# Performance work log

Measured on AMD Instinct MI355X. Metric: run time of the kernel, lower is better.

## Reference

```python
import jax, jax.numpy as jnp
import numpy as np

H = 16        # num query heads
HKV = 4       # num kv heads
D = 128       # head_dim
HID = 2048    # hidden_size
G = H // HKV  # heads per kv group


def setup_inputs() -> dict:
    key = jax.random.key(0)
    ks = jax.random.split(key, 9)
    s = 0.02
    x = jax.random.normal(ks[0], (2, 2048, HID), dtype=jnp.float32)
    wq = jax.random.normal(ks[1], (HID, H * D), dtype=jnp.float32) * s
    bq = jnp.zeros((H * D,), jnp.float32)
    wk = jax.random.normal(ks[2], (HID, HKV * D), dtype=jnp.float32) * s
    bk = jnp.zeros((HKV * D,), jnp.float32)
    wv = jax.random.normal(ks[3], (HID, HKV * D), dtype=jnp.float32) * s
    bv = jnp.zeros((HKV * D,), jnp.float32)
    wo = jax.random.normal(ks[4], (HID, HID), dtype=jnp.float32) * s
    bo = jnp.zeros((HID,), jnp.float32)
    return dict(x=x, wq=wq, bq=bq, wk=wk, bk=bk, wv=wv, bv=bv, wo=wo, bo=bo)


def reference(x, wq, bq, wk, bk, wv, bv, wo, bo):
    B, S, _ = x.shape
    scale = jnp.float32(1.0 / np.sqrt(D))
    # projections (torch Linear with weight stored as [in, out] here)
    q = (x @ wq + bq).reshape(B, S, H, D)          # [B,S,H,D]
    k = (x @ wk + bk).reshape(B, S, HKV, D)        # [B,S,Hkv,D]
    v = (x @ wv + bv).reshape(B, S, HKV, D)
    # group query heads by kv head instead of expanding KV
    q = q.reshape(B, S, HKV, G, D)
    scores = jnp.einsum('bqhgd,bkhd->bhgqk', q, k) * scale  # [B,Hkv,G,S,S]
    causal = jnp.triu(jnp.ones((S, S), dtype=bool), k=1)
    scores = jnp.where(causal, jnp.float32(-1e9), scores)
    weights = jax.nn.softmax(scores, axis=-1)
    out = jnp.einsum('bhgqk,bkhd->bqhgd', weights, v)        # [B,S,Hkv,G,D]
    out = out.reshape(B, S, H * D)
    return out @ wo + bo
```

## Files before the change

kernel.cpp:

```cpp
#include <hip/hip_runtime.h>
#include <hip/hip_bf16.h>
#include <math.h>

#define HID 2048
#define NH 16
#define NKV 4
#define HD 128
#define GQ 4
#define BATCH 2

typedef short short8v __attribute__((ext_vector_type(8)));
typedef float f32x4 __attribute__((ext_vector_type(4)));

__device__ __forceinline__ ushort f2bf(float f) {
  uint u = __float_as_uint(f);
  uint r = (u + 0x7fffu + ((u >> 16) & 1u)) >> 16;
  return (ushort)r;
}

__device__ __forceinline__ void gld_lds16(const void* g, void* lds) {
  __builtin_amdgcn_global_load_lds(
      (const __attribute__((address_space(1))) unsigned int*)g,
      (__attribute__((address_space(3))) unsigned int*)lds, 16, 0, 0);
}

#define WAVE_LDS_FENCE()                                \
  do {                                                  \
    asm volatile("s_waitcnt lgkmcnt(0)" ::: "memory");  \
    __builtin_amdgcn_sched_barrier(0);                  \
  } while (0)

__device__ const int QT_TAB[24] = {7, 8, 9, 10, 11, 12, 13, 14, 15, 15, 6, 14,
                                   5, 13, 4, 12, 3, 11, 2, 10, 1, 9, 0, 8};
__device__ const int LO_TAB[24] = {0, 0, 0, 0, 0, 0, 0, 0, 0, 16, 0, 16,
                                   0, 16, 0, 16, 0, 16, 0, 16, 0, 16, 0, 16};

__global__ __launch_bounds__(256) void castx_kernel(
    const float* __restrict__ x, ushort* __restrict__ xb) {
  const int i = ((int)blockIdx.x * 256 + (int)threadIdx.x) * 8;
  float4 f0 = *reinterpret_cast<const float4*>(x + i);
  float4 f1 = *reinterpret_cast<const float4*>(x + i + 4);
  uint4 o;
  o.x = (uint)f2bf(f0.x) | ((uint)f2bf(f0.y) << 16);
  o.y = (uint)f2bf(f0.z) | ((uint)f2bf(f0.w) << 16);
  o.z = (uint)f2bf(f1.x) | ((uint)f2bf(f1.y) << 16);
  o.w = (uint)f2bf(f1.z) | ((uint)f2bf(f1.w) << 16);
  *reinterpret_cast<uint4*>(xb + i) = o;
}

__global__ __launch_bounds__(256) void tcast_kernel(
    const float* __restrict__ W, ushort* __restrict__ Wt, int K, int N) {
  __shared__ float T[32][33];
  const int k0 = blockIdx.x * 32;
  const int n0 = blockIdx.y * 32;
  const int t = threadIdx.x;
  const int r = t >> 3;
  const int c4 = (t & 7) * 4;
  float4 vin = *reinterpret_cast<const float4*>(
      &W[(size_t)(k0 + r) * N + n0 + c4]);
  T[c4 + 0][r] = vin.x;
  T[c4 + 1][r] = vin.y;
  T[c4 + 2][r] = vin.z;
  T[c4 + 3][r] = vin.w;
  __syncthreads();
  ushort4 o;
  o.x = f2bf(T[r][c4 + 0]);
  o.y = f2bf(T[r][c4 + 1]);
  o.z = f2bf(T[r][c4 + 2]);
  o.w = f2bf(T[r][c4 + 3]);
  *reinterpret_cast<ushort4*>(&Wt[(size_t)(n0 + r) * K + k0 + c4]) = o;
}

__global__ __launch_bounds__(256) void zero_kernel(float4* __restrict__ p) {
  p[(size_t)blockIdx.x * 256 + threadIdx.x] = (float4){0.f, 0.f, 0.f, 0.f};
}

__global__ __launch_bounds__(256) void merge_kernel(
    const float* __restrict__ Oacc, const float* __restrict__ Lacc,
    ushort* __restrict__ attnb) {
  const int i = (int)blockIdx.x * 256 + (int)threadIdx.x;
  const int d8 = i & 15;
  const int h = (i >> 4) & 15;
  const int r = i >> 8;
  const float invl = 1.0f / Lacc[r * NH + h];
  const float* src = Oacc + ((size_t)r * (NH * HD)) + h * HD + d8 * 8;
  float4 a0 = *reinterpret_cast<const float4*>(src);
  float4 a1 = *reinterpret_cast<const float4*>(src + 4);
  uint4 o;
  o.x = (uint)f2bf(a0.x * invl) | ((uint)f2bf(a0.y * invl) << 16);
  o.y = (uint)f2bf(a0.z * invl) | ((uint)f2bf(a0.w * invl) << 16);
  o.z = (uint)f2bf(a1.x * invl) | ((uint)f2bf(a1.y * invl) << 16);
  o.w = (uint)f2bf(a1.z * invl) | ((uint)f2bf(a1.w * invl) << 16);
  const int b = r >> 10;
  const int s = 1024 + (r & 1023);
  *reinterpret_cast<uint4*>(
      &attnb[((size_t)(b * 2048 + s)) * (NH * HD) + h * HD + d8 * 8]) = o;
}

template <int MODE>
__global__ __launch_bounds__(256) void gemm_big(
    const ushort* __restrict__ A,
    const ushort* __restrict__ W0, const ushort* __restrict__ W1,
    const ushort* __restrict__ W2,
    const float* __restrict__ b0, const float* __restrict__ b1,
    const float* __restrict__ b2,
    void* __restrict__ C0, void* __restrict__ C1, void* __restrict__ C2,
    int M, int K, int S) {
  __shared__ ushort As[2][128 * 32];
  __shared__ ushort Bs[2][128 * 32];
  const int tid = threadIdx.x;
  const int m0 = blockIdx.y * 128;
  const int n0 = blockIdx.x * 128;
  const int wave = tid >> 6;
  const int lane = tid & 63;
  const int quad = lane >> 4;
  const int lr = lane & 15;
  const int l4 = lane >> 2;
  const int lc = (lane & 3) * 8;
  const int wm = (wave >> 1) * 64;
  const int wn = (wave & 1) * 64;

  const ushort* Wt;
  const float* bias;
  int nloc, Nout, om;
  void* Cout;
  if (MODE == 0) {
    Wt = W0; bias = b0; nloc = n0; Nout = 2048; om = 0; Cout = C0;
  } else {
    if (n0 < 2048)      { Wt = W0; bias = b0; nloc = n0;        Nout = 2048; om = 1; Cout = C0; }
    else if (n0 < 2560) { Wt = W1; bias = b1; nloc = n0 - 2048; Nout = 512;  om = 1; Cout = C1; }
    else                { Wt = W2; bias = b2; nloc = n0 - 2560; Nout = 512;  om = 2; Cout = C2; }
  }

  f32x4 acc[4][4];
#pragma unroll
  for (int i = 0; i < 4; ++i)
#pragma unroll
    for (int j = 0; j < 4; ++j) acc[i][j] = (f32x4){0.f, 0.f, 0.f, 0.f};

  const size_t rowA = (size_t)(m0 + wave * 32 + l4) * K + lc;
  const size_t rowB = (size_t)(nloc + wave * 32 + l4) * K + lc;

#define STAGE_GEMM(t, bi)                                                  \
  do {                                                                     \
    const int kof = (t) * 32;                                              \
    gld_lds16(&A[rowA + kof], &As[bi][(wave * 32) * 32]);                  \
    gld_lds16(&A[rowA + 16 * K + kof], &As[bi][(wave * 32 + 16) * 32]);    \
    gld_lds16(&Wt[rowB + kof], &Bs[bi][(wave * 32) * 32]);                 \
    gld_lds16(&Wt[rowB + 16 * K + kof], &Bs[bi][(wave * 32 + 16) * 32]);   \
  } while (0)

  const int nt = K / 32;
  STAGE_GEMM(0, 0);

  for (int t = 0; t < nt; ++t) {
    const int cur = t & 1;
    __builtin_amdgcn_s_barrier();
    if (t + 1 < nt) {
      STAGE_GEMM(t + 1, cur ^ 1);
      asm volatile("s_waitcnt vmcnt(4)" ::: "memory");
    } else {
      asm volatile("s_waitcnt vmcnt(0)" ::: "memory");
    }
    __builtin_amdgcn_s_barrier();
    __builtin_amdgcn_sched_barrier(0);

    short8v af[4], bf[4];
#pragma unroll
    for (int x = 0; x < 4; ++x) {
      const int ra = wm + x * 16 + lr;
      af[x] = *reinterpret_cast<const short8v*>(&As[cur][ra * 32 + quad * 8]);
      const int rb = wn + x * 16 + lr;
      bf[x] = *reinterpret_cast<const short8v*>(&Bs[cur][rb * 32 + quad * 8]);
    }
#pragma unroll
    for (int i = 0; i < 4; ++i)
#pragma unroll
      for (int j = 0; j < 4; ++j)
        acc[i][j] = __builtin_amdgcn_mfma_f32_16x16x32_bf16(
            af[i], bf[j], acc[i][j], 0, 0, 0);
  }
#undef STAGE_GEMM

#pragma unroll
  for (int i = 0; i < 4; ++i) {
    const int row_base = m0 + wm + i * 16 + quad * 4;
#pragma unroll
    for (int j = 0; j < 4; ++j) {
      const int col = nloc + wn + j * 16 + lr;
      const float b = bias[col];
      if (om == 0) {
        float* C = (float*)Cout;
#pragma unroll
        for (int rg = 0; rg < 4; ++rg)
          C[(size_t)(row_base + rg) * Nout + col] = acc[i][j][rg] + b;
      } else if (om == 1) {
        ushort* C = (ushort*)Cout;
#pragma unroll
        for (int rg = 0; rg < 4; ++rg)
          C[(size_t)(row_base + rg) * Nout + col] = f2bf(acc[i][j][rg] + b);
      } else {
        ushort* C = (ushort*)Cout;
        const int bb = (row_base >= S) ? 1 : 0;
        const int s = row_base - bb * S;
        const int kvh = col >> 7;
        const int d = col & 127;
        ushort4 o;
        o.x = f2bf(acc[i][j][0] + b);
        o.y = f2bf(acc[i][j][1] + b);
        o.z = f2bf(acc[i][j][2] + b);
        o.w = f2bf(acc[i][j][3] + b);
        *reinterpret_cast<ushort4*>(
            &C[((size_t)(bb * NKV + kvh) * HD + d) * S + s]) = o;
      }
    }
  }
}

__device__ __forceinline__ void stage_kv_dma8(
    const ushort* __restrict__ Kb, const ushort* __restrict__ Vb,
    ushort* Kdst, ushort* Vdst, int k0, int S, int wave, int lane) {
  const int rK = lane >> 4, cK = lane & 15;
  const int rV = lane >> 3, cV = lane & 7;
#pragma unroll
  for (int c = 0; c < 2; ++c) {
    const int g = wave * 2 + c;
    const int row = g * 4 + rK;
    const int jk = cK ^ (row & 15);
    gld_lds16(&Kb[(size_t)(k0 + row) * (NKV * HD) + jk * 8], &Kdst[g * 512]);
    const int d = g * 8 + rV;
    const int jv = cV ^ (d & 7);
    gld_lds16(&Vb[(size_t)d * S + k0 + jv * 8], &Vdst[g * 512]);
  }
}

__global__ __launch_bounds__(512, 4) void gqa_attn_mfma(
    const ushort* __restrict__ Qg, const ushort* __restrict__ Kgl,
    const ushort* __restrict__ Vt_g, ushort* __restrict__ O,
    float* __restrict__ Oacc, float* __restrict__ Lacc, int S) {
  __shared__ __align__(16) ushort L[32768];
  ushort* K0 = L;
  ushort* K1 = L + 8192;
  ushort* V0 = L + 16384;
  ushort* V1 = L + 24576;

  const int tid = threadIdx.x;
  const int wave = tid >> 6;
  const int lane = tid & 63;
  const int quad = lane >> 4;
  const int lr = lane & 15;
  const int item = blockIdx.z;
  const int qt = QT_TAB[item];
  const int lo = LO_TAB[item];
  const int ntf = 2 * qt + 2;
  const int hi = lo ? ntf : (ntf < 16 ? ntf : 16);
  const bool part = (qt >= 8);
  const int q0 = qt * 128;
  const int hq = blockIdx.x;
  const int b = blockIdx.y;
  const int kvh = hq >> 2;
  const float scale = 0.08838834764831845f;

  const ushort* Qb = Qg + ((size_t)b * S) * (NH * HD) + (size_t)hq * HD;
  const ushort* Kb = Kgl + ((size_t)b * S) * (NKV * HD) + (size_t)kvh * HD;
  const ushort* Vb = Vt_g + ((size_t)(b * NKV + kvh) * HD) * S;

#pragma unroll
  for (int i = 0; i < 4; ++i) {
    const int id = tid + i * 512;
    const int r = id >> 4, c = id & 15;
    const int p = c ^ (r & 15);
    *reinterpret_cast<uint4*>(&L[r * 128 + p * 8]) =
        *reinterpret_cast<const uint4*>(
            &Qb[(size_t)(q0 + r) * (NH * HD) + c * 8]);
  }
  __syncthreads();
  short8v aq[4];
  {
    const int ra = wave * 16 + lr;
#pragma unroll
    for (int ks = 0; ks < 4; ++ks)
      aq[ks] = *reinterpret_cast<const short8v*>(
          &L[ra * 128 + (((ks * 4 + quad) ^ lr) & 15) * 8]);
  }
  __syncthreads();

  f32x4 oacc[8];
#pragma unroll
  for (int nb = 0; nb < 8; ++nb) oacc[nb] = (f32x4){0.f, 0.f, 0.f, 0.f};
  float l_r = 0.f;

  const int laneA = ((quad * 2) & 3) * 16 + lr;
  const int laneB = ((quad * 2 + 1) & 3) * 16 + lr;
  const bool hihalf = (quad >= 2);

  stage_kv_dma8(Kb, Vb, (lo & 1) ? K1 : K0, (lo & 1) ? V1 : V0, lo * 64, S,
                wave, lane);

  for (int kt = lo; kt < hi; ++kt) {
    const int k0 = kt * 64;
    const ushort* Kc = (kt & 1) ? K1 : K0;
    const ushort* Vc = (kt & 1) ? V1 : V0;

    __builtin_amdgcn_s_barrier();
    if (kt + 1 < hi) {
      ushort* Kn = (kt & 1) ? K0 : K1;
      ushort* Vn = (kt & 1) ? V0 : V1;
      stage_kv_dma8(Kb, Vb, Kn, Vn, k0 + 64, S, wave, lane);
      asm volatile("s_waitcnt vmcnt(4)" ::: "memory");
    } else {
      asm volatile("s_waitcnt vmcnt(0)" ::: "memory");
    }
    __builtin_amdgcn_s_barrier();
    __builtin_amdgcn_sched_barrier(0);

    f32x4 sacc[4];
    __builtin_amdgcn_s_setprio(1);
#pragma unroll
    for (int nb = 0; nb < 4; ++nb) {
      sacc[nb] = (f32x4){0.f, 0.f, 0.f, 0.f};
      const int rb = nb * 16 + lr;
#pragma unroll
      for (int ks = 0; ks < 4; ++ks) {
        short8v bk = *reinterpret_cast<const short8v*>(
            &Kc[rb * 128 + (((ks * 4 + quad) ^ lr) & 15) * 8]);
        sacc[nb] = __builtin_amdgcn_mfma_f32_16x16x32_bf16(
            bk, aq[ks], sacc[nb], 0, 0, 0);
      }
    }
    __builtin_amdgcn_s_setprio(0);

    const bool needmask = (kt >= 2 * qt);
    const int qi = q0 + wave * 16 + lr;
    uint u[4][2];
    float rs = 0.f;
#pragma unroll
    for (int nb = 0; nb < 4; ++nb) {
      float p[4];
#pragma unroll
      for (int rg = 0; rg < 4; ++rg) {
        float sv = sacc[nb][rg] * scale;
        if (needmask) {
          const int kj = k0 + nb * 16 + quad * 4 + rg;
          if (kj > qi) sv = -1e30f;
        }
        p[rg] = __expf(sv);
        rs += p[rg];
      }
      u[nb][0] = (uint)f2bf(p[0]) | ((uint)f2bf(p[1]) << 16);
      u[nb][1] = (uint)f2bf(p[2]) | ((uint)f2bf(p[3]) << 16);
    }
    rs += __shfl_xor(rs, 16);
    rs += __shfl_xor(rs, 32);
    l_r += rs;

    short8v ap[2];
#pragma unroll
    for (int ks = 0; ks < 2; ++ks) {
      const uint w0a = __shfl(u[2 * ks + 0][0], laneA);
      const uint w0b = __shfl(u[2 * ks + 1][0], laneA);
      const uint w1a = __shfl(u[2 * ks + 0][1], laneA);
      const uint w1b = __shfl(u[2 * ks + 1][1], laneA);
      const uint w2a = __shfl(u[2 * ks + 0][0], laneB);
      const uint w2b = __shfl(u[2 * ks + 1][0], laneB);
      const uint w3a = __shfl(u[2 * ks + 0][1], laneB);
      const uint w3b = __shfl(u[2 * ks + 1][1], laneB);
      uint4 q4;
      q4.x = hihalf ? w0b : w0a;
      q4.y = hihalf ? w1b : w1a;
      q4.z = hihalf ? w2b : w2a;
      q4.w = hihalf ? w3b : w3a;
      ap[ks] = *reinterpret_cast<short8v*>(&q4);
    }

    __builtin_amdgcn_s_setprio(1);
#pragma unroll
    for (int nb = 0; nb < 8; ++nb) {
      const int rv = nb * 16 + lr;
#pragma unroll
      for (int ks = 0; ks < 2; ++ks) {
        short8v bv = *reinterpret_cast<const short8v*>(
            &Vc[rv * 64 + (((ks * 4 + quad) ^ lr) & 7) * 8]);
        oacc[nb] = __builtin_amdgcn_mfma_f32_16x16x32_bf16(
            ap[ks], bv, oacc[nb], 0, 0, 0);
      }
    }
    __builtin_amdgcn_s_setprio(0);
  }

  if (part) {
    float* Oa = Oacc +
                ((size_t)(b * 1024 + (q0 - 1024) + wave * 16 + quad * 4)) *
                    (NH * HD) +
                hq * HD;
#pragma unroll
    for (int nb = 0; nb < 8; ++nb)
#pragma unroll
      for (int rg = 0; rg < 4; ++rg)
        atomicAdd(&Oa[(size_t)rg * (NH * HD) + nb * 16 + lr], oacc[nb][rg]);
    if (quad == 0)
      atomicAdd(
          &Lacc[(size_t)(b * 1024 + (q0 - 1024) + wave * 16 + lr) * NH + hq],
          l_r);
  } else {
    const float invl = 1.0f / l_r;
    float inv[4];
#pragma unroll
    for (int rg = 0; rg < 4; ++rg)
      inv[rg] = __shfl(invl, (lane & 48) | (quad * 4 + rg));
    __syncthreads();
    ushort* ow = &L[wave * 16 * 128];
#pragma unroll
    for (int nb = 0; nb < 8; ++nb)
#pragma unroll
      for (int rg = 0; rg < 4; ++rg)
        ow[(quad * 4 + rg) * 128 + nb * 16 + lr] =
            f2bf(oacc[nb][rg] * inv[rg]);
    WAVE_LDS_FENCE();
    ushort* Ob = O + ((size_t)b * S) * (NH * HD) + (size_t)hq * HD;
#pragma unroll
    for (int ii = 0; ii < 4; ++ii) {
      const int id = lane + ii * 64;
      const int r16 = id >> 4, c = id & 15;
      uint4 val = *reinterpret_cast<const uint4*>(&ow[r16 * 128 + c * 8]);
      *reinterpret_cast<uint4*>(
          &Ob[(size_t)(q0 + wave * 16 + r16) * (NH * HD) + c * 8]) = val;
    }
  }
}

extern "C" void kernel_launch(void* const* d_in, const int* in_sizes, int n_in,
                              void* d_out, int out_size, void* d_ws,
                              size_t ws_size, hipStream_t stream) {
  const float* x = (const float*)d_in[0];
  const float* wq = (const float*)d_in[1];
  const float* bq = (const float*)d_in[2];
  const float* wk = (const float*)d_in[3];
  const float* bk = (const float*)d_in[4];
  const float* wv = (const float*)d_in[5];
  const float* bv = (const float*)d_in[6];
  const float* wo = (const float*)d_in[7];
  const float* bo = (const float*)d_in[8];
  float* out = (float*)d_out;

  const int M = in_sizes[0] / HID;
  const int S = M / BATCH;

  char* w = (char*)d_ws;
  ushort* xb    = (ushort*)(w + 0);
  ushort* qb    = (ushort*)(w + (16u << 20));
  ushort* kb    = (ushort*)(w + (32u << 20));
  ushort* vT    = (ushort*)(w + (36u << 20));
  ushort* attnb = (ushort*)(w + (40u << 20));
  ushort* wqT   = (ushort*)(w + (56u << 20));
  ushort* wkT   = (ushort*)(w + (64u << 20));
  ushort* wvT   = (ushort*)(w + (66u << 20));
  ushort* woT   = (ushort*)(w + (68u << 20));
  float* Oacc = (float*)(w + 0);
  float* Lacc = (float*)(w + (64u << 20));

  dim3 blk(256);
  castx_kernel<<<dim3((M * HID) / (8 * 256)), blk, 0, stream>>>(x, xb);
  tcast_kernel<<<dim3(HID / 32, (NH * HD) / 32), blk, 0, stream>>>(
      wq, wqT, HID, NH * HD);
  tcast_kernel<<<dim3(HID / 32, (NKV * HD) / 32), blk, 0, stream>>>(
      wk, wkT, HID, NKV * HD);
  tcast_kernel<<<dim3(HID / 32, (NKV * HD) / 32), blk, 0, stream>>>(
      wv, wvT, HID, NKV * HD);
  tcast_kernel<<<dim3(HID / 32, HID / 32), blk, 0, stream>>>(
      wo, woT, HID, HID);

  gemm_big<1><<<dim3(3072 / 128, M / 128), blk, 0, stream>>>(
      xb, wqT, wkT, wvT, bq, bk, bv, qb, kb, vT, M, HID, S);

  zero_kernel<<<dim3(4096), blk, 0, stream>>>((float4*)Oacc);
  zero_kernel<<<dim3(32), blk, 0, stream>>>((float4*)Lacc);

  gqa_attn_mfma<<<dim3(NH, BATCH, 24), dim3(512), 0, stream>>>(
      qb, kb, vT, attnb, Oacc, Lacc, S);

  merge_kernel<<<dim3(2048), blk, 0, stream>>>(Oacc, Lacc, attnb);

  gemm_big<0><<<dim3(HID / 128, M / 128), blk, 0, stream>>>(
      attnb, woT, nullptr, nullptr, bo, nullptr, nullptr,
      out, nullptr, nullptr, M, HID, S);
}
```

Before: 330.9 us.

## Split partial attention buffers to drop atomics and zeroing, single-buffer V for occupancy

Each of the two key-range partial blocks now writes plain stores into its own O/L buffer instead of atomically adding into one shared buffer. The second buffer reuses the output tensor as scratch, which removes both zero-fill kernels, and the merge kernel sums the two partials. The V tile is single-buffered and loaded just in time behind a second barrier, so LDS per block shrinks and the launch-bounds target rises from 4 to 6 blocks per CU. The exponent switches to exp2 with a folded log2e scale and bf16 packing uses a hardware pack instruction. The costs are V load latency that is no longer hidden by a prefetch, an extra barrier per tile, and a dependence on the output buffer being free until the final GEMM.

```diff
diff --git a/kernel.cpp b/kernel.cpp
--- a/kernel.cpp
+++ b/kernel.cpp
@@ -16,6 +16,12 @@
   uint u = __float_as_uint(f);
   uint r = (u + 0x7fffu + ((u >> 16) & 1u)) >> 16;
   return (ushort)r;
+}
+
+__device__ __forceinline__ uint cvt_pk_bf16(float lo, float hi) {
+  uint r;
+  asm("v_cvt_pk_bf16_f32 %0, %1, %2" : "=v"(r) : "v"(lo), "v"(hi));
+  return r;
 }
 
 __device__ __forceinline__ void gld_lds16(const void* g, void* lds) {
@@ -71,26 +77,25 @@
   *reinterpret_cast<ushort4*>(&Wt[(size_t)(n0 + r) * K + k0 + c4]) = o;
 }
 
-__global__ __launch_bounds__(256) void zero_kernel(float4* __restrict__ p) {
-  p[(size_t)blockIdx.x * 256 + threadIdx.x] = (float4){0.f, 0.f, 0.f, 0.f};
-}
-
 __global__ __launch_bounds__(256) void merge_kernel(
-    const float* __restrict__ Oacc, const float* __restrict__ Lacc,
+    const float* __restrict__ OaccA, const float* __restrict__ OaccB,
+    const float* __restrict__ LaccA, const float* __restrict__ LaccB,
     ushort* __restrict__ attnb) {
   const int i = (int)blockIdx.x * 256 + (int)threadIdx.x;
   const int d8 = i & 15;
   const int h = (i >> 4) & 15;
   const int r = i >> 8;
-  const float invl = 1.0f / Lacc[r * NH + h];
-  const float* src = Oacc + ((size_t)r * (NH * HD)) + h * HD + d8 * 8;
-  float4 a0 = *reinterpret_cast<const float4*>(src);
-  float4 a1 = *reinterpret_cast<const float4*>(src + 4);
+  const float invl = 1.0f / (LaccA[r * NH + h] + LaccB[r * NH + h]);
+  const size_t off = ((size_t)r * (NH * HD)) + h * HD + d8 * 8;
+  float4 a0 = *reinterpret_cast<const float4*>(OaccA + off);
+  float4 a1 = *reinterpret_cast<const float4*>(OaccA + off + 4);
+  float4 b0 = *reinterpret_cast<const float4*>(OaccB + off);
+  float4 b1 = *reinterpret_cast<const float4*>(OaccB + off + 4);
   uint4 o;
-  o.x = (uint)f2bf(a0.x * invl) | ((uint)f2bf(a0.y * invl) << 16);
-  o.y = (uint)f2bf(a0.z * invl) | ((uint)f2bf(a0.w * invl) << 16);
-  o.z = (uint)f2bf(a1.x * invl) | ((uint)f2bf(a1.y * invl) << 16);
-  o.w = (uint)f2bf(a1.z * invl) | ((uint)f2bf(a1.w * invl) << 16);
+  o.x = cvt_pk_bf16((a0.x + b0.x) * invl, (a0.y + b0.y) * invl);
+  o.y = cvt_pk_bf16((a0.z + b0.z) * invl, (a0.w + b0.w) * invl);
+  o.z = cvt_pk_bf16((a1.x + b1.x) * invl, (a1.y + b1.y) * invl);
+  o.w = cvt_pk_bf16((a1.z + b1.z) * invl, (a1.w + b1.w) * invl);
   const int b = r >> 10;
   const int s = 1024 + (r & 1023);
   *reinterpret_cast<uint4*>(
@@ -217,32 +222,40 @@
   }
 }
 
-__device__ __forceinline__ void stage_kv_dma8(
-    const ushort* __restrict__ Kb, const ushort* __restrict__ Vb,
-    ushort* Kdst, ushort* Vdst, int k0, int S, int wave, int lane) {
+__device__ __forceinline__ void stage_k8(const ushort* __restrict__ Kb,
+                                         ushort* Kdst, int k0, int wave,
+                                         int lane) {
   const int rK = lane >> 4, cK = lane & 15;
-  const int rV = lane >> 3, cV = lane & 7;
 #pragma unroll
   for (int c = 0; c < 2; ++c) {
     const int g = wave * 2 + c;
     const int row = g * 4 + rK;
     const int jk = cK ^ (row & 15);
     gld_lds16(&Kb[(size_t)(k0 + row) * (NKV * HD) + jk * 8], &Kdst[g * 512]);
+  }
+}
+__device__ __forceinline__ void stage_v8(const ushort* __restrict__ Vb,
+                                         ushort* Vdst, int k0, int S, int wave,
+                                         int lane) {
+  const int rV = lane >> 3, cV = lane & 7;
+#pragma unroll
+  for (int c = 0; c < 2; ++c) {
+    const int g = wave * 2 + c;
     const int d = g * 8 + rV;
     const int jv = cV ^ (d & 7);
     gld_lds16(&Vb[(size_t)d * S + k0 + jv * 8], &Vdst[g * 512]);
   }
 }
 
-__global__ __launch_bounds__(512, 4) void gqa_attn_mfma(
+__global__ __launch_bounds__(512, 6) void gqa_attn_mfma(
     const ushort* __restrict__ Qg, const ushort* __restrict__ Kgl,
     const ushort* __restrict__ Vt_g, ushort* __restrict__ O,
-    float* __restrict__ Oacc, float* __restrict__ Lacc, int S) {
-  __shared__ __align__(16) ushort L[32768];
+    float* __restrict__ OaccA, float* __restrict__ OaccB,
+    float* __restrict__ LaccA, float* __restrict__ LaccB, int S) {
+  __shared__ __align__(16) ushort L[24576];
   ushort* K0 = L;
   ushort* K1 = L + 8192;
-  ushort* V0 = L + 16384;
-  ushort* V1 = L + 24576;
+  ushort* Vs = L + 16384;
 
   const int tid = threadIdx.x;
   const int wave = tid >> 6;
@@ -259,7 +272,7 @@
   const int hq = blockIdx.x;
   const int b = blockIdx.y;
   const int kvh = hq >> 2;
-  const float scale = 0.08838834764831845f;
+  const float C = 0.12751745f;
 
   const ushort* Qb = Qg + ((size_t)b * S) * (NH * HD) + (size_t)hq * HD;
   const ushort* Kb = Kgl + ((size_t)b * S) * (NKV * HD) + (size_t)kvh * HD;
@@ -294,22 +307,19 @@
   const int laneB = ((quad * 2 + 1) & 3) * 16 + lr;
   const bool hihalf = (quad >= 2);
 
-  stage_kv_dma8(Kb, Vb, (lo & 1) ? K1 : K0, (lo & 1) ? V1 : V0, lo * 64, S,
-                wave, lane);
+  stage_k8(Kb, (lo & 1) ? K1 : K0, lo * 64, wave, lane);
 
   for (int kt = lo; kt < hi; ++kt) {
-    const int k0 = kt * 64;
+    const int k0v = kt * 64;
     const ushort* Kc = (kt & 1) ? K1 : K0;
-    const ushort* Vc = (kt & 1) ? V1 : V0;
 
     __builtin_amdgcn_s_barrier();
+    stage_v8(Vb, Vs, k0v, S, wave, lane);
     if (kt + 1 < hi) {
-      ushort* Kn = (kt & 1) ? K0 : K1;
-      ushort* Vn = (kt & 1) ? V0 : V1;
-      stage_kv_dma8(Kb, Vb, Kn, Vn, k0 + 64, S, wave, lane);
+      stage_k8(Kb, (kt & 1) ? K0 : K1, k0v + 64, wave, lane);
       asm volatile("s_waitcnt vmcnt(4)" ::: "memory");
     } else {
-      asm volatile("s_waitcnt vmcnt(0)" ::: "memory");
+      asm volatile("s_waitcnt vmcnt(2)" ::: "memory");
     }
     __builtin_amdgcn_s_barrier();
     __builtin_amdgcn_sched_barrier(0);
@@ -339,16 +349,16 @@
       float p[4];
 #pragma unroll
       for (int rg = 0; rg < 4; ++rg) {
-        float sv = sacc[nb][rg] * scale;
+        float sv = sacc[nb][rg] * C;
         if (needmask) {
-          const int kj = k0 + nb * 16 + quad * 4 + rg;
+          const int kj = k0v + nb * 16 + quad * 4 + rg;
           if (kj > qi) sv = -1e30f;
         }
-        p[rg] = __expf(sv);
+        p[rg] = __builtin_amdgcn_exp2f(sv);
         rs += p[rg];
       }
-      u[nb][0] = (uint)f2bf(p[0]) | ((uint)f2bf(p[1]) << 16);
-      u[nb][1] = (uint)f2bf(p[2]) | ((uint)f2bf(p[3]) << 16);
+      u[nb][0] = cvt_pk_bf16(p[0], p[1]);
+      u[nb][1] = cvt_pk_bf16(p[2], p[3]);
     }
     rs += __shfl_xor(rs, 16);
     rs += __shfl_xor(rs, 32);
@@ -373,6 +383,14 @@
       ap[ks] = *reinterpret_cast<short8v*>(&q4);
     }
 
+    if (kt + 1 < hi) {
+      asm volatile("s_waitcnt vmcnt(2)" ::: "memory");
+    } else {
+      asm volatile("s_waitcnt vmcnt(0)" ::: "memory");
+    }
+    __builtin_amdgcn_s_barrier();
+    __builtin_amdgcn_sched_barrier(0);
+
     __builtin_amdgcn_s_setprio(1);
 #pragma unroll
     for (int nb = 0; nb < 8; ++nb) {
@@ -380,7 +398,7 @@
 #pragma unroll
       for (int ks = 0; ks < 2; ++ks) {
         short8v bv = *reinterpret_cast<const short8v*>(
-            &Vc[rv * 64 + (((ks * 4 + quad) ^ lr) & 7) * 8]);
+            &Vs[rv * 64 + (((ks * 4 + quad) ^ lr) & 7) * 8]);
         oacc[nb] = __builtin_amdgcn_mfma_f32_16x16x32_bf16(
             ap[ks], bv, oacc[nb], 0, 0, 0);
       }
@@ -389,6 +407,8 @@
   }
 
   if (part) {
+    float* Oacc = lo ? OaccB : OaccA;
+    float* Lacc = lo ? LaccB : LaccA;
     float* Oa = Oacc +
                 ((size_t)(b * 1024 + (q0 - 1024) + wave * 16 + quad * 4)) *
                     (NH * HD) +
@@ -397,11 +417,9 @@
     for (int nb = 0; nb < 8; ++nb)
 #pragma unroll
       for (int rg = 0; rg < 4; ++rg)
-        atomicAdd(&Oa[(size_t)rg * (NH * HD) + nb * 16 + lr], oacc[nb][rg]);
+        Oa[(size_t)rg * (NH * HD) + nb * 16 + lr] = oacc[nb][rg];
     if (quad == 0)
-      atomicAdd(
-          &Lacc[(size_t)(b * 1024 + (q0 - 1024) + wave * 16 + lr) * NH + hq],
-          l_r);
+      Lacc[(size_t)(b * 1024 + (q0 - 1024) + wave * 16 + lr) * NH + hq] = l_r;
   } else {
     const float invl = 1.0f / l_r;
     float inv[4];
@@ -456,8 +474,10 @@
   ushort* wkT   = (ushort*)(w + (64u << 20));
   ushort* wvT   = (ushort*)(w + (66u << 20));
   ushort* woT   = (ushort*)(w + (68u << 20));
-  float* Oacc = (float*)(w + 0);
-  float* Lacc = (float*)(w + (64u << 20));
+  float* OaccA = (float*)(w + 0);
+  float* OaccB = out;
+  float* LaccA = (float*)(w + (64u << 20));
+  float* LaccB = (float*)(w + (66u << 20));
 
   dim3 blk(256);
   castx_kernel<<<dim3((M * HID) / (8 * 256)), blk, 0, stream>>>(x, xb);
@@ -473,13 +493,11 @@
   gemm_big<1><<<dim3(3072 / 128, M / 128), blk, 0, stream>>>(
       xb, wqT, wkT, wvT, bq, bk, bv, qb, kb, vT, M, HID, S);
 
-  zero_kernel<<<dim3(4096), blk, 0, stream>>>((float4*)Oacc);
-  zero_kernel<<<dim3(32), blk, 0, stream>>>((float4*)Lacc);
-
   gqa_attn_mfma<<<dim3(NH, BATCH, 24), dim3(512), 0, stream>>>(
-      qb, kb, vT, attnb, Oacc, Lacc, S);
-
-  merge_kernel<<<dim3(2048), blk, 0, stream>>>(Oacc, Lacc, attnb);
+      qb, kb, vT, attnb, OaccA, OaccB, LaccA, LaccB, S);
+
+  merge_kernel<<<dim3(2048), blk, 0, stream>>>(
+      OaccA, OaccB, LaccA, LaccB, attnb);
 
   gemm_big<0><<<dim3(HID / 128, M / 128), blk, 0, stream>>>(
       attnb, woT, nullptr, nullptr, bo, nullptr, nullptr,
```

Measured after the change: 348.8 us. 1.05x slower.
